# Kernel tuning notes

Measured on AMD Instinct MI355X. Metric: run time of the kernel, lower is better.

Reference implementation:

```python
import jax, jax.numpy as jnp
import numpy as np

STRIDES = (8, 16, 32)
BINS = 16
NC = 80
ALPHA, GAMMA = 0.25, 2.0
W_CLS, W_IOU, W_DFL = 1.0, 7.5, 1.5
B, MAX_GT = 32, 32
EPS = 1e-7


def setup_inputs() -> dict:
    key = jax.random.key(0)
    k0, k1, k2, k3, k4, k5, k6 = jax.random.split(key, 7)
    p0 = jax.random.normal(k0, (B, 4 * BINS + NC, 80, 80), dtype=jnp.float32)
    p1 = jax.random.normal(k1, (B, 4 * BINS + NC, 40, 40), dtype=jnp.float32)
    p2 = jax.random.normal(k2, (B, 4 * BINS + NC, 20, 20), dtype=jnp.float32)
    # realistic xyxy boxes inside a 640x640 image
    c = jax.random.uniform(k3, (B, MAX_GT, 2), minval=60.0, maxval=580.0)
    wh = jax.random.uniform(k4, (B, MAX_GT, 2), minval=16.0, maxval=120.0)
    gt_bboxes = jnp.concatenate([c - wh / 2, c + wh / 2], axis=-1).astype(jnp.float32)
    gt_labels = jax.random.randint(k5, (B, MAX_GT), 0, NC, dtype=jnp.int32)
    raw = jax.random.randint(k6, (B, 8400), 0, 20 * MAX_GT, dtype=jnp.int32)
    matched_gt_inds = jnp.where(raw < MAX_GT, raw, -1)
    return {"p0": p0, "p1": p1, "p2": p2, "gt_bboxes": gt_bboxes,
            "gt_labels": gt_labels, "matched_gt_inds": matched_gt_inds}


def _decode_scale(p, stride):
    # p: [B, 4*BINS + NC, H, W]
    Bp, C, H, W = p.shape
    dfl = p[:, :4 * BINS].reshape(Bp, 4, BINS, H, W)
    cls = p[:, 4 * BINS:]
    # DFL decode: expectation of softmax over bins, scaled by stride
    prob = jax.nn.softmax(dfl, axis=2)
    proj = jnp.arange(BINS, dtype=p.dtype)
    dist = jnp.einsum('bkchw,c->bkhw', prob, proj) * stride  # [B,4,H,W] in pixels
    ys, xs = jnp.meshgrid(jnp.arange(H), jnp.arange(W), indexing='ij')
    cx = ((xs.astype(p.dtype)) + 0.5) * stride
    cy = ((ys.astype(p.dtype)) + 0.5) * stride
    boxes = jnp.stack([cx - dist[:, 0], cy - dist[:, 1],
                       cx + dist[:, 2], cy + dist[:, 3]], axis=-1).reshape(Bp, H * W, 4)
    cls_logits = cls.transpose(0, 2, 3, 1).reshape(Bp, H * W, NC)
    dfl_flat = dfl.transpose(0, 3, 4, 1, 2).reshape(Bp, H * W, 4, BINS)
    grid = jnp.stack([cx, cy], axis=-1).reshape(H * W, 2)
    smap = jnp.full((H * W,), stride, dtype=p.dtype)
    return cls_logits, dfl_flat, boxes, grid, smap


def reference(p0, p1, p2, gt_bboxes, gt_labels, matched_gt_inds):
    outs = [_decode_scale(p, s) for p, s in zip((p0, p1, p2), STRIDES)]
    scores = jnp.concatenate([o[0] for o in outs], axis=1)   # [B,N,NC]
    dfl = jnp.concatenate([o[1] for o in outs], axis=1)      # [B,N,4,BINS]
    pboxes = jnp.concatenate([o[2] for o in outs], axis=1)   # [B,N,4]
    grid = jnp.concatenate([o[3] for o in outs], axis=0)     # [N,2]
    smap = jnp.concatenate([o[4] for o in outs], axis=0)     # [N]

    pos = matched_gt_inds >= 0                               # [B,N]
    idx = jnp.where(pos, matched_gt_inds, 0)
    lbl = jnp.take_along_axis(gt_labels, idx, axis=1)        # [B,N]
    posf = pos.astype(scores.dtype)
    tgt_scores = jax.nn.one_hot(lbl, NC, dtype=scores.dtype) * posf[..., None]

    # sigmoid focal loss (stable BCE-with-logits)
    prob = jax.nn.sigmoid(scores)
    ce = jnp.maximum(scores, 0) - scores * tgt_scores + jnp.log1p(jnp.exp(-jnp.abs(scores)))
    p_t = prob * tgt_scores + (1 - prob) * (1 - tgt_scores)
    alpha_t = tgt_scores * ALPHA + (1 - tgt_scores) * (1 - ALPHA)
    cls_elem = alpha_t * (1.0 - p_t) ** GAMMA * ce
    num_pos = jnp.maximum(posf.sum(), 1.0)
    loss_cls = cls_elem.sum() / num_pos

    # gather matched GT boxes per anchor
    tboxes = jnp.take_along_axis(gt_bboxes, idx[..., None], axis=1)  # [B,N,4]
    gx, gy = grid[None, :, 0], grid[None, :, 1]
    l = jnp.clip(gx - tboxes[..., 0], 0.0)
    t = jnp.clip(gy - tboxes[..., 1], 0.0)
    r = jnp.clip(tboxes[..., 2] - gx, 0.0)
    b_ = jnp.clip(tboxes[..., 3] - gy, 0.0)
    dists = jnp.stack([l, t, r, b_], axis=-1) / smap[None, :, None]   # [B,N,4]
    tb = jnp.clip(dists, 0.0, BINS - 1 - 1e-6)
    lo = jnp.floor(tb).astype(jnp.int32)
    hi = jnp.minimum(lo + 1, BINS - 1)
    a = tb - lo.astype(tb.dtype)
    # soft two-bin DFL target (vectorized form of the scatter_add loop)
    tdist = (jax.nn.one_hot(lo, BINS, dtype=dfl.dtype) * (1.0 - a)[..., None]
             + jax.nn.one_hot(hi, BINS, dtype=dfl.dtype) * a[..., None])   # [B,N,4,BINS]
    logp = jax.nn.log_softmax(dfl, axis=-1)
    dfl_elem = -(tdist * logp).sum(-1)                                # [B,N,4]
    loss_dfl = (dfl_elem * posf[..., None]).sum() / (num_pos * 4.0)

    # IoU loss on positives
    ix1 = jnp.maximum(pboxes[..., 0], tboxes[..., 0])
    iy1 = jnp.maximum(pboxes[..., 1], tboxes[..., 1])
    ix2 = jnp.minimum(pboxes[..., 2], tboxes[..., 2])
    iy2 = jnp.minimum(pboxes[..., 3], tboxes[..., 3])
    inter = jnp.clip(ix2 - ix1, 0.0) * jnp.clip(iy2 - iy1, 0.0)
    area_p = jnp.clip(pboxes[..., 2] - pboxes[..., 0], 0.0) * jnp.clip(pboxes[..., 3] - pboxes[..., 1], 0.0)
    area_t = jnp.clip(tboxes[..., 2] - tboxes[..., 0], 0.0) * jnp.clip(tboxes[..., 3] - tboxes[..., 1], 0.0)
    iou = inter / (area_p + area_t - inter + EPS)
    loss_iou = ((1.0 - iou) * posf).sum() / num_pos

    total = W_CLS * loss_cls + W_IOU * loss_iou + W_DFL * loss_dfl
    return total
```

## Files before the change

kernel.cpp:

```cpp
#include <hip/hip_runtime.h>
#include <math.h>

#define NCLS 80
#define BINS 16
#define BATCH 32
#define MAX_GT 32
#define NA 8400
#define AN (BATCH * NA)
#define NT 2100
#define NB_DFL 1050
#define NB_CLS 2560
#define NVB (NB_DFL + NB_CLS)
#define GRID 2048
#define NSLOT 64
#define ALPHA_C 0.25f
#define W_CLS 1.0
#define W_IOU 7.5
#define W_DFL 1.5
#define EPS_F 1e-7f

__device__ __forceinline__ float focal_elem(float s, float tt)
{
    float e   = __expf(-fabsf(s));
    float inv = 1.f / (1.f + e);
    float prob = (s >= 0.f) ? inv : e * inv;
    float ce  = fmaxf(s, 0.f) - s * tt + __logf(1.f + e);
    float p_t = prob * tt + (1.f - prob) * (1.f - tt);
    float alpha_t = tt * ALPHA_C + (1.f - tt) * (1.f - ALPHA_C);
    float om = 1.f - p_t;
    return alpha_t * om * om * ce;
}

__device__ __forceinline__ float focal0(float s)
{
    float e   = __expf(-fabsf(s));
    float inv = 1.f / (1.f + e);
    float prob = (s >= 0.f) ? inv : e * inv;
    float sp  = fmaxf(s, 0.f) + __logf(1.f + e);
    return 0.75f * prob * prob * sp;
}

__device__ __forceinline__ void block_write4(float c0, float c1, float c2, float c3,
                                             double* __restrict__ blk)
{
    #pragma unroll
    for (int o = 32; o > 0; o >>= 1) {
        c0 += __shfl_down(c0, o);
        c1 += __shfl_down(c1, o);
        c2 += __shfl_down(c2, o);
        c3 += __shfl_down(c3, o);
    }
    __shared__ float s4[4][4];
    const int wave = threadIdx.x >> 6, lane = threadIdx.x & 63;
    if (lane == 0) { s4[wave][0] = c0; s4[wave][1] = c1; s4[wave][2] = c2; s4[wave][3] = c3; }
    __syncthreads();
    if (threadIdx.x == 0) {
        double* o = blk + (size_t)blockIdx.x * 4;
        o[0] = (double)(s4[0][0] + s4[1][0] + s4[2][0] + s4[3][0]);
        o[1] = (double)(s4[0][1] + s4[1][1] + s4[2][1] + s4[3][1]);
        o[2] = (double)(s4[0][2] + s4[1][2] + s4[2][2] + s4[3][2]);
        o[3] = (double)(s4[0][3] + s4[1][3] + s4[2][3] + s4[3][3]);
    }
}

template<int HW, int SSTR, int WQ>
__device__ __forceinline__ void dfl_scale(
    const float* __restrict__ p, int b, int tl, int k, int gbase, int tid,
    const float* __restrict__ gt_bboxes, const int* __restrict__ gt_labels,
    const int* __restrict__ matched,
    float& c_cls, float& c_iou, float& c_dfl, float& c_cnt)
{
    const float stride = (float)SSTR;
    const float inv_s  = 1.f / stride;
    const int h  = tl / WQ;
    const int w0 = (tl - h * WQ) * 4;
    const int off = tl * 4;
    const float cy = ((float)h + 0.5f) * stride;
    const float* pc = p + (size_t)(b * 144 + k * BINS) * HW + off;

    const int4 m4 = *(const int4*)(matched + (size_t)b * NA + gbase + off);
    const int mm[4] = {m4.x, m4.y, m4.z, m4.w};

    float se[4] = {0.f, 0.f, 0.f, 0.f}, we[4] = {0.f, 0.f, 0.f, 0.f};
    #pragma unroll
    for (int i0 = 0; i0 < BINS; i0 += 4) {
        float4 qv[4];
        #pragma unroll
        for (int r = 0; r < 4; ++r)
            qv[r] = *(const float4*)(pc + (size_t)((i0 + r) * HW));
        #pragma unroll
        for (int r = 0; r < 4; ++r) {
            const float wgt = (float)(i0 + r);
            float e0 = __expf(qv[r].x), e1 = __expf(qv[r].y);
            float e2 = __expf(qv[r].z), e3 = __expf(qv[r].w);
            se[0] += e0; we[0] = fmaf(wgt, e0, we[0]);
            se[1] += e1; we[1] = fmaf(wgt, e1, we[1]);
            se[2] += e2; we[2] = fmaf(wgt, e2, we[2]);
            se[3] += e3; we[3] = fmaf(wgt, e3, we[3]);
        }
    }

    float pd[4];
    #pragma unroll
    for (int j = 0; j < 4; ++j) pd[j] = (we[j] / se[j]) * stride;

    #pragma unroll
    for (int j = 0; j < 4; ++j) {
        if (mm[j] >= 0) {
            const float4 tb = *(const float4*)(gt_bboxes + ((size_t)b * MAX_GT + mm[j]) * 4);
            const float cx = ((float)(w0 + j) + 0.5f) * stride;
            float d = (k == 0) ? (cx - tb.x) : (k == 1) ? (cy - tb.y)
                    : (k == 2) ? (tb.z - cx) : (tb.w - cy);
            float tval = fminf(fmaxf(d, 0.f) * inv_s, (float)(BINS - 1) - 1e-6f);
            int   lo = (int)tval;
            float fr = tval - (float)lo;
            float vlo = pc[(size_t)(lo * HW) + 0];
            float vhi = pc[(size_t)((lo + 1) * HW) + 0];
            vlo = pc[(size_t)(lo * HW) + j];
            vhi = pc[(size_t)((lo + 1) * HW) + j];
            float lse = __logf(se[j]);
            c_dfl += -((1.f - fr) * (vlo - lse) + fr * (vhi - lse));
        }
    }

    const int lbase = (tid & 63) & ~3;
    float d1[4], d2[4], d3[4];
    #pragma unroll
    for (int j = 0; j < 4; ++j) {
        d1[j] = __shfl(pd[j], lbase + 1);
        d2[j] = __shfl(pd[j], lbase + 2);
        d3[j] = __shfl(pd[j], lbase + 3);
    }
    if (k == 0) {
        #pragma unroll
        for (int j = 0; j < 4; ++j) {
            if (mm[j] >= 0) {
                const float cx = ((float)(w0 + j) + 0.5f) * stride;
                float px1 = cx - pd[j], py1 = cy - d1[j];
                float px2 = cx + d2[j], py2 = cy + d3[j];
                const float4 tb = *(const float4*)(gt_bboxes + ((size_t)b * MAX_GT + mm[j]) * 4);
                float ix1 = fmaxf(px1, tb.x), iy1 = fmaxf(py1, tb.y);
                float ix2 = fminf(px2, tb.z), iy2 = fminf(py2, tb.w);
                float inter  = fmaxf(ix2 - ix1, 0.f) * fmaxf(iy2 - iy1, 0.f);
                float area_p = fmaxf(px2 - px1, 0.f) * fmaxf(py2 - py1, 0.f);
                float area_t = fmaxf(tb.z - tb.x, 0.f) * fmaxf(tb.w - tb.y, 0.f);
                float iou = inter / (area_p + area_t - inter + EPS_F);
                c_iou += 1.f - iou;
                c_cnt += 1.f;
                int lbl = gt_labels[b * MAX_GT + mm[j]];
                float sv = *(p + (size_t)(b * 144 + 4 * BINS + lbl) * HW + off + j);
                c_cls += focal_elem(sv, 1.f) - focal_elem(sv, 0.f);
            }
        }
    }
}

__device__ __forceinline__ void cls_unit(int cvb, int tid,
    const float* __restrict__ p0, const float* __restrict__ p1,
    const float* __restrict__ p2, float& c_cls)
{
    const int b = cvb / NCLS;
    const int c = cvb - b * NCLS;
    const size_t cls_ch = (size_t)(b * 144 + 4 * BINS + c);

    float4 q[9];
    const float* pl0 = p0 + cls_ch * 6400;
    #pragma unroll
    for (int i = 0; i < 6; ++i) {
        int off = (i * 256 + tid) * 4;
        q[i] = *(const float4*)(pl0 + off);
    }
    #pragma unroll
    for (int i = 6; i < 9; ++i) {
        int t  = i * 256 + tid;
        int tc = (t < NT) ? t : 0;
        const float* p; int HW, off;
        if (tc < 1600)      { p = p0; HW = 6400; off = tc * 4; }
        else if (tc < 2000) { p = p1; HW = 1600; off = (tc - 1600) * 4; }
        else                { p = p2; HW = 400;  off = (tc - 2000) * 4; }
        q[i] = *(const float4*)(p + cls_ch * HW + off);
    }

    float part = 0.f;
    #pragma unroll
    for (int i = 0; i < 9; ++i) {
        const bool valid = (i < 8) || (i * 256 + tid < NT);
        float sum = focal0(q[i].x) + focal0(q[i].y) + focal0(q[i].z) + focal0(q[i].w);
        part += valid ? sum : 0.f;
    }
    c_cls += part;
}

__global__ __launch_bounds__(256) void yolo_mega(
    const float* __restrict__ p0, const float* __restrict__ p1, const float* __restrict__ p2,
    const float* __restrict__ gt_bboxes, const int* __restrict__ gt_labels,
    const int* __restrict__ matched, double* __restrict__ blk)
{
    const int tid = (int)threadIdx.x;
    float c_cls = 0.f, c_iou = 0.f, c_dfl = 0.f, c_cnt = 0.f;

    for (int vb = (int)blockIdx.x; vb < NVB; vb += GRID) {
        if (vb < NB_DFL) {
            const int gdt = vb * 256 + tid;
            const int k   = gdt & 3;
            const int qg  = gdt >> 2;
            const int b   = qg / NT;
            const int t   = qg - b * NT;
            if (t < 1600)
                dfl_scale<6400,  8, 20>(p0, b, t,        k, 0,    tid,
                                        gt_bboxes, gt_labels, matched, c_cls, c_iou, c_dfl, c_cnt);
            else if (t < 2000)
                dfl_scale<1600, 16, 10>(p1, b, t - 1600, k, 6400, tid,
                                        gt_bboxes, gt_labels, matched, c_cls, c_iou, c_dfl, c_cnt);
            else
                dfl_scale< 400, 32,  5>(p2, b, t - 2000, k, 8000, tid,
                                        gt_bboxes, gt_labels, matched, c_cls, c_iou, c_dfl, c_cnt);
        } else {
            cls_unit(vb - NB_DFL, tid, p0, p1, p2, c_cls);
        }
    }
    block_write4(c_cls, c_iou, c_dfl, c_cnt, blk);
}

__global__ __launch_bounds__(1024) void yolo_finalize_blocks(
    const double* __restrict__ blk, float* __restrict__ out)
{
    const int tid = (int)threadIdx.x;
    const double2* r0 = (const double2*)(blk + (size_t)tid * 4);
    const double2* r1 = (const double2*)(blk + (size_t)(tid + 1024) * 4);
    double2 a0 = r0[0], a1 = r0[1], b0 = r1[0], b1 = r1[1];
    double s0 = a0.x + b0.x, s1 = a0.y + b0.y, s2 = a1.x + b1.x, s3 = a1.y + b1.y;
    #pragma unroll
    for (int o = 32; o > 0; o >>= 1) {
        s0 += __shfl_down(s0, o); s1 += __shfl_down(s1, o);
        s2 += __shfl_down(s2, o); s3 += __shfl_down(s3, o);
    }
    __shared__ double sh[16][4];
    const int wave = tid >> 6, lane = tid & 63;
    if (lane == 0) { sh[wave][0] = s0; sh[wave][1] = s1; sh[wave][2] = s2; sh[wave][3] = s3; }
    __syncthreads();
    if (tid == 0) {
        double c = 0, i = 0, d = 0, n = 0;
        for (int w = 0; w < 16; ++w) { c += sh[w][0]; i += sh[w][1]; d += sh[w][2]; n += sh[w][3]; }
        double np = (n < 1.0) ? 1.0 : n;
        out[0] = (float)(W_CLS * c / np + W_IOU * i / np + W_DFL * d / (np * 4.0));
    }
}

__device__ __forceinline__ void block_reduce_atomic(float val, double* __restrict__ target)
{
    __shared__ float s[4];
    __syncthreads();
    #pragma unroll
    for (int o = 32; o > 0; o >>= 1) val += __shfl_down(val, o);
    const int wave = threadIdx.x >> 6, lane = threadIdx.x & 63;
    if (lane == 0) s[wave] = val;
    __syncthreads();
    if (threadIdx.x == 0) atomicAdd(target, (double)(s[0] + s[1] + s[2] + s[3]));
}

__global__ __launch_bounds__(256) void yolo_loss_fused(
    const float* __restrict__ p0, const float* __restrict__ p1, const float* __restrict__ p2,
    const float* __restrict__ gt_bboxes, const int* __restrict__ gt_labels,
    const int* __restrict__ matched, double* __restrict__ acc)
{
    const int a = blockIdx.x * blockDim.x + threadIdx.x;
    const int b = blockIdx.y;
    const int slot = blockIdx.x & (NSLOT - 1);
    float cls_acc = 0.f, iou_acc = 0.f, dfl_acc = 0.f, pos_cnt = 0.f;
    if (a < NA) {
        const float* p; int HW, W; float stride; int off;
        if (a < 6400)      { p = p0; HW = 6400; W = 80; stride = 8.f;  off = a; }
        else if (a < 8000) { p = p1; HW = 1600; W = 40; stride = 16.f; off = a - 6400; }
        else               { p = p2; HW = 400;  W = 20; stride = 32.f; off = a - 8000; }
        const int h = off / W, w = off - h * W;
        const float cx = ((float)w + 0.5f) * stride, cy = ((float)h + 0.5f) * stride;
        const float* pb = p + ((size_t)b * 144) * (size_t)HW + (size_t)off;
        const int m = matched[(size_t)b * NA + a];
        const bool pos = (m >= 0);
        const int idx = pos ? m : 0;
        const int lbl = gt_labels[b * MAX_GT + idx];
        const float* tbp = gt_bboxes + ((size_t)b * MAX_GT + idx) * 4;
        const float tx1 = tbp[0], ty1 = tbp[1], tx2 = tbp[2], ty2 = tbp[3];
        float tdist[4] = {fmaxf(cx - tx1, 0.f) / stride, fmaxf(cy - ty1, 0.f) / stride,
                          fmaxf(tx2 - cx, 0.f) / stride, fmaxf(ty2 - cy, 0.f) / stride};
        float pdv[4]; float dfl_sum = 0.f;
        #pragma unroll
        for (int k = 0; k < 4; ++k) {
            float tv = fminf(tdist[k], (float)(BINS - 1) - 1e-6f);
            int lo = (int)floorf(tv);
            float fr = tv - (float)lo;
            const float* pcx = pb + (size_t)(k * BINS) * HW;
            float v[BINS];
            #pragma unroll
            for (int i = 0; i < BINS; ++i) v[i] = pcx[(size_t)i * HW];
            float mx = v[0];
            #pragma unroll
            for (int i = 1; i < BINS; ++i) mx = fmaxf(mx, v[i]);
            float se = 0.f, we = 0.f, vlo = 0.f, vhi = 0.f;
            #pragma unroll
            for (int i = 0; i < BINS; ++i) {
                float e = __expf(v[i] - mx);
                se += e; we += (float)i * e;
                vlo = (i == lo) ? v[i] : vlo;
                vhi = (i == lo + 1) ? v[i] : vhi;
            }
            pdv[k] = (we / se) * stride;
            if (pos) { float lse = mx + __logf(se); dfl_sum += -((1.f - fr) * (vlo - lse) + fr * (vhi - lse)); }
        }
        const float* pcls = pb + (size_t)(4 * BINS) * HW;
        #pragma unroll 4
        for (int c = 0; c < NCLS; ++c)
            cls_acc += focal_elem(pcls[(size_t)c * HW], (pos && c == lbl) ? 1.f : 0.f);
        if (pos) {
            float px1 = cx - pdv[0], py1 = cy - pdv[1], px2 = cx + pdv[2], py2 = cy + pdv[3];
            float ix1 = fmaxf(px1, tx1), iy1 = fmaxf(py1, ty1);
            float ix2 = fminf(px2, tx2), iy2 = fminf(py2, ty2);
            float inter  = fmaxf(ix2 - ix1, 0.f) * fmaxf(iy2 - iy1, 0.f);
            float area_p = fmaxf(px2 - px1, 0.f) * fmaxf(py2 - py1, 0.f);
            float area_t = fmaxf(tx2 - tx1, 0.f) * fmaxf(ty2 - ty1, 0.f);
            float iou = inter / (area_p + area_t - inter + EPS_F);
            iou_acc = 1.f - iou; dfl_acc = dfl_sum; pos_cnt = 1.f;
        }
    }
    block_reduce_atomic(cls_acc, &acc[0 * NSLOT + slot]);
    block_reduce_atomic(iou_acc, &acc[1 * NSLOT + slot]);
    block_reduce_atomic(dfl_acc, &acc[2 * NSLOT + slot]);
    block_reduce_atomic(pos_cnt, &acc[3 * NSLOT + slot]);
}

__global__ void yolo_loss_finalize(const double* __restrict__ acc, float* __restrict__ out)
{
    double s[4] = {0.0, 0.0, 0.0, 0.0};
    for (int q = 0; q < 4; ++q)
        for (int i = 0; i < NSLOT; ++i) s[q] += acc[q * NSLOT + i];
    double np = s[3] < 1.0 ? 1.0 : s[3];
    double total = W_CLS * s[0] / np + W_IOU * s[1] / np + W_DFL * s[2] / (np * 4.0);
    out[0] = (float)total;
}

extern "C" void kernel_launch(void* const* d_in, const int* in_sizes, int n_in,
                              void* d_out, int out_size, void* d_ws, size_t ws_size,
                              hipStream_t stream)
{
    const float* p0        = (const float*)d_in[0];
    const float* p1        = (const float*)d_in[1];
    const float* p2        = (const float*)d_in[2];
    const float* gt_bboxes = (const float*)d_in[3];
    const int*   gt_labels = (const int*)d_in[4];
    const int*   matched   = (const int*)d_in[5];
    float*  out = (float*)d_out;

    const size_t need = (size_t)GRID * 4 * sizeof(double);

    if (ws_size >= need) {
        double* blk = (double*)d_ws;
        yolo_mega<<<GRID, 256, 0, stream>>>(p0, p1, p2, gt_bboxes, gt_labels, matched, blk);
        yolo_finalize_blocks<<<1, 1024, 0, stream>>>(blk, out);
    } else {
        double* acc = (double*)d_ws;
        (void)hipMemsetAsync(acc, 0, 4 * NSLOT * sizeof(double), stream);
        dim3 g((NA + 255) / 256, BATCH);
        yolo_loss_fused<<<g, 256, 0, stream>>>(p0, p1, p2, gt_bboxes, gt_labels, matched, acc);
        yolo_loss_finalize<<<1, 1, 0, stream>>>(acc, out);
    }
}
```

Before: 216.8 us.

## Restructure mega kernel to 128-thread blocks with contiguous class chunks and per-wave partials

```diff
diff --git a/kernel.cpp b/kernel.cpp
--- a/kernel.cpp
+++ b/kernel.cpp
@@ -8,10 +8,11 @@
 #define NA 8400
 #define AN (BATCH * NA)
 #define NT 2100
-#define NB_DFL 1050
-#define NB_CLS 2560
-#define NVB (NB_DFL + NB_CLS)
 #define GRID 2048
+#define NU_DFL 2100
+#define NU_CLS 5280
+#define NVB (NU_DFL + NU_CLS)
+#define NROWS (GRID * 2)
 #define NSLOT 64
 #define ALPHA_C 0.25f
 #define W_CLS 1.0
@@ -19,29 +20,26 @@
 #define W_DFL 1.5
 #define EPS_F 1e-7f
 
-__device__ __forceinline__ float focal_elem(float s, float tt)
-{
-    float e   = __expf(-fabsf(s));
-    float inv = 1.f / (1.f + e);
-    float prob = (s >= 0.f) ? inv : e * inv;
-    float ce  = fmaxf(s, 0.f) - s * tt + __logf(1.f + e);
-    float p_t = prob * tt + (1.f - prob) * (1.f - tt);
-    float alpha_t = tt * ALPHA_C + (1.f - tt) * (1.f - ALPHA_C);
-    float om = 1.f - p_t;
-    return alpha_t * om * om * ce;
-}
-
 __device__ __forceinline__ float focal0(float s)
 {
-    float e   = __expf(-fabsf(s));
-    float inv = 1.f / (1.f + e);
-    float prob = (s >= 0.f) ? inv : e * inv;
-    float sp  = fmaxf(s, 0.f) + __logf(1.f + e);
-    return 0.75f * prob * prob * sp;
-}
-
-__device__ __forceinline__ void block_write4(float c0, float c1, float c2, float c3,
-                                             double* __restrict__ blk)
+    float e  = __expf(-s);
+    float t  = 1.f + e;
+    float r  = __builtin_amdgcn_rcpf(t);
+    float lg = __logf(t);
+    return 0.75f * r * r * (s + lg);
+}
+
+__device__ __forceinline__ float focal_corr(float s)
+{
+    float e  = __expf(-s);
+    float t  = 1.f + e;
+    float r  = __builtin_amdgcn_rcpf(t);
+    float lg = __logf(t);
+    return r * r * (0.25f * e * e * lg - 0.75f * (s + lg));
+}
+
+__device__ __forceinline__ void wave_write4(float c0, float c1, float c2, float c3,
+                                            double* __restrict__ blk)
 {
     #pragma unroll
     for (int o = 32; o > 0; o >>= 1) {
@@ -50,16 +48,11 @@
         c2 += __shfl_down(c2, o);
         c3 += __shfl_down(c3, o);
     }
-    __shared__ float s4[4][4];
-    const int wave = threadIdx.x >> 6, lane = threadIdx.x & 63;
-    if (lane == 0) { s4[wave][0] = c0; s4[wave][1] = c1; s4[wave][2] = c2; s4[wave][3] = c3; }
-    __syncthreads();
-    if (threadIdx.x == 0) {
-        double* o = blk + (size_t)blockIdx.x * 4;
-        o[0] = (double)(s4[0][0] + s4[1][0] + s4[2][0] + s4[3][0]);
-        o[1] = (double)(s4[0][1] + s4[1][1] + s4[2][1] + s4[3][1]);
-        o[2] = (double)(s4[0][2] + s4[1][2] + s4[2][2] + s4[3][2]);
-        o[3] = (double)(s4[0][3] + s4[1][3] + s4[2][3] + s4[3][3]);
+    const int lane = (int)threadIdx.x & 63;
+    if (lane == 0) {
+        const int row = (int)blockIdx.x * 2 + ((int)threadIdx.x >> 6);
+        double* o = blk + (size_t)row * 4;
+        o[0] = (double)c0; o[1] = (double)c1; o[2] = (double)c2; o[3] = (double)c3;
     }
 }
 
@@ -78,26 +71,23 @@
     const float cy = ((float)h + 0.5f) * stride;
     const float* pc = p + (size_t)(b * 144 + k * BINS) * HW + off;
 
+    float4 v[BINS];
+    #pragma unroll
+    for (int i = 0; i < BINS; ++i)
+        v[i] = *(const float4*)(pc + (size_t)(i * HW));
     const int4 m4 = *(const int4*)(matched + (size_t)b * NA + gbase + off);
     const int mm[4] = {m4.x, m4.y, m4.z, m4.w};
 
     float se[4] = {0.f, 0.f, 0.f, 0.f}, we[4] = {0.f, 0.f, 0.f, 0.f};
     #pragma unroll
-    for (int i0 = 0; i0 < BINS; i0 += 4) {
-        float4 qv[4];
-        #pragma unroll
-        for (int r = 0; r < 4; ++r)
-            qv[r] = *(const float4*)(pc + (size_t)((i0 + r) * HW));
-        #pragma unroll
-        for (int r = 0; r < 4; ++r) {
-            const float wgt = (float)(i0 + r);
-            float e0 = __expf(qv[r].x), e1 = __expf(qv[r].y);
-            float e2 = __expf(qv[r].z), e3 = __expf(qv[r].w);
-            se[0] += e0; we[0] = fmaf(wgt, e0, we[0]);
-            se[1] += e1; we[1] = fmaf(wgt, e1, we[1]);
-            se[2] += e2; we[2] = fmaf(wgt, e2, we[2]);
-            se[3] += e3; we[3] = fmaf(wgt, e3, we[3]);
-        }
+    for (int i = 0; i < BINS; ++i) {
+        const float wgt = (float)i;
+        float e0 = __expf(v[i].x), e1 = __expf(v[i].y);
+        float e2 = __expf(v[i].z), e3 = __expf(v[i].w);
+        se[0] += e0; we[0] = fmaf(wgt, e0, we[0]);
+        se[1] += e1; we[1] = fmaf(wgt, e1, we[1]);
+        se[2] += e2; we[2] = fmaf(wgt, e2, we[2]);
+        se[3] += e3; we[3] = fmaf(wgt, e3, we[3]);
     }
 
     float pd[4];
@@ -114,10 +104,8 @@
             float tval = fminf(fmaxf(d, 0.f) * inv_s, (float)(BINS - 1) - 1e-6f);
             int   lo = (int)tval;
             float fr = tval - (float)lo;
-            float vlo = pc[(size_t)(lo * HW) + 0];
-            float vhi = pc[(size_t)((lo + 1) * HW) + 0];
-            vlo = pc[(size_t)(lo * HW) + j];
-            vhi = pc[(size_t)((lo + 1) * HW) + j];
+            float vlo = pc[(size_t)(lo * HW) + j];
+            float vhi = pc[(size_t)((lo + 1) * HW) + j];
             float lse = __logf(se[j]);
             c_dfl += -((1.f - fr) * (vlo - lse) + fr * (vhi - lse));
         }
@@ -149,49 +137,13 @@
                 c_cnt += 1.f;
                 int lbl = gt_labels[b * MAX_GT + mm[j]];
                 float sv = *(p + (size_t)(b * 144 + 4 * BINS + lbl) * HW + off + j);
-                c_cls += focal_elem(sv, 1.f) - focal_elem(sv, 0.f);
+                c_cls += focal_corr(sv);
             }
         }
     }
 }
 
-__device__ __forceinline__ void cls_unit(int cvb, int tid,
-    const float* __restrict__ p0, const float* __restrict__ p1,
-    const float* __restrict__ p2, float& c_cls)
-{
-    const int b = cvb / NCLS;
-    const int c = cvb - b * NCLS;
-    const size_t cls_ch = (size_t)(b * 144 + 4 * BINS + c);
-
-    float4 q[9];
-    const float* pl0 = p0 + cls_ch * 6400;
-    #pragma unroll
-    for (int i = 0; i < 6; ++i) {
-        int off = (i * 256 + tid) * 4;
-        q[i] = *(const float4*)(pl0 + off);
-    }
-    #pragma unroll
-    for (int i = 6; i < 9; ++i) {
-        int t  = i * 256 + tid;
-        int tc = (t < NT) ? t : 0;
-        const float* p; int HW, off;
-        if (tc < 1600)      { p = p0; HW = 6400; off = tc * 4; }
-        else if (tc < 2000) { p = p1; HW = 1600; off = (tc - 1600) * 4; }
-        else                { p = p2; HW = 400;  off = (tc - 2000) * 4; }
-        q[i] = *(const float4*)(p + cls_ch * HW + off);
-    }
-
-    float part = 0.f;
-    #pragma unroll
-    for (int i = 0; i < 9; ++i) {
-        const bool valid = (i < 8) || (i * 256 + tid < NT);
-        float sum = focal0(q[i].x) + focal0(q[i].y) + focal0(q[i].z) + focal0(q[i].w);
-        part += valid ? sum : 0.f;
-    }
-    c_cls += part;
-}
-
-__global__ __launch_bounds__(256) void yolo_mega(
+__global__ __launch_bounds__(128, 4) void yolo_mega(
     const float* __restrict__ p0, const float* __restrict__ p1, const float* __restrict__ p2,
     const float* __restrict__ gt_bboxes, const int* __restrict__ gt_labels,
     const int* __restrict__ matched, double* __restrict__ blk)
@@ -200,8 +152,8 @@
     float c_cls = 0.f, c_iou = 0.f, c_dfl = 0.f, c_cnt = 0.f;
 
     for (int vb = (int)blockIdx.x; vb < NVB; vb += GRID) {
-        if (vb < NB_DFL) {
-            const int gdt = vb * 256 + tid;
+        if (vb < NU_DFL) {
+            const int gdt = vb * 128 + tid;
             const int k   = gdt & 3;
             const int qg  = gdt >> 2;
             const int b   = qg / NT;
@@ -216,20 +168,44 @@
                 dfl_scale< 400, 32,  5>(p2, b, t - 2000, k, 8000, tid,
                                         gt_bboxes, gt_labels, matched, c_cls, c_iou, c_dfl, c_cnt);
         } else {
-            cls_unit(vb - NB_DFL, tid, p0, p1, p2, c_cls);
-        }
-    }
-    block_write4(c_cls, c_iou, c_dfl, c_cnt, blk);
+            const int c = vb - NU_DFL;
+            const int b = c / 165;
+            const int r = c - b * 165;
+            const float* base; int len, off;
+            if (r < 125)      { base = p0 + (size_t)b * 921600 + 409600; len = 512000; off = r * 4096; }
+            else if (r < 157) { base = p1 + (size_t)b * 230400 + 102400; len = 128000; off = (r - 125) * 4096; }
+            else              { base = p2 + (size_t)b * 57600  + 25600;  len = 32000;  off = (r - 157) * 4096; }
+
+            float4 q[8]; bool val[8];
+            #pragma unroll
+            for (int i = 0; i < 8; ++i) {
+                int o = off + i * 512 + tid * 4;
+                val[i] = (o < len);
+                q[i] = *(const float4*)(base + (val[i] ? o : 0));
+            }
+            float part = 0.f;
+            #pragma unroll
+            for (int i = 0; i < 8; ++i) {
+                float s = focal0(q[i].x) + focal0(q[i].y) + focal0(q[i].z) + focal0(q[i].w);
+                part += val[i] ? s : 0.f;
+            }
+            c_cls += part;
+        }
+    }
+    wave_write4(c_cls, c_iou, c_dfl, c_cnt, blk);
 }
 
 __global__ __launch_bounds__(1024) void yolo_finalize_blocks(
     const double* __restrict__ blk, float* __restrict__ out)
 {
     const int tid = (int)threadIdx.x;
-    const double2* r0 = (const double2*)(blk + (size_t)tid * 4);
-    const double2* r1 = (const double2*)(blk + (size_t)(tid + 1024) * 4);
-    double2 a0 = r0[0], a1 = r0[1], b0 = r1[0], b1 = r1[1];
-    double s0 = a0.x + b0.x, s1 = a0.y + b0.y, s2 = a1.x + b1.x, s3 = a1.y + b1.y;
+    double s0 = 0.0, s1 = 0.0, s2 = 0.0, s3 = 0.0;
+    #pragma unroll
+    for (int r = tid; r < NROWS; r += 1024) {
+        const double2* rp = (const double2*)(blk + (size_t)r * 4);
+        double2 a = rp[0], b = rp[1];
+        s0 += a.x; s1 += a.y; s2 += b.x; s3 += b.y;
+    }
     #pragma unroll
     for (int o = 32; o > 0; o >>= 1) {
         s0 += __shfl_down(s0, o); s1 += __shfl_down(s1, o);
@@ -257,6 +233,18 @@
     if (lane == 0) s[wave] = val;
     __syncthreads();
     if (threadIdx.x == 0) atomicAdd(target, (double)(s[0] + s[1] + s[2] + s[3]));
+}
+
+__device__ __forceinline__ float focal_elem(float s, float tt)
+{
+    float e   = __expf(-fabsf(s));
+    float inv = 1.f / (1.f + e);
+    float prob = (s >= 0.f) ? inv : e * inv;
+    float ce  = fmaxf(s, 0.f) - s * tt + __logf(1.f + e);
+    float p_t = prob * tt + (1.f - prob) * (1.f - tt);
+    float alpha_t = tt * ALPHA_C + (1.f - tt) * (1.f - ALPHA_C);
+    float om = 1.f - p_t;
+    return alpha_t * om * om * ce;
 }
 
 __global__ __launch_bounds__(256) void yolo_loss_fused(
@@ -351,11 +339,11 @@
     const int*   matched   = (const int*)d_in[5];
     float*  out = (float*)d_out;
 
-    const size_t need = (size_t)GRID * 4 * sizeof(double);
+    const size_t need = (size_t)NROWS * 4 * sizeof(double);
 
     if (ws_size >= need) {
         double* blk = (double*)d_ws;
-        yolo_mega<<<GRID, 256, 0, stream>>>(p0, p1, p2, gt_bboxes, gt_labels, matched, blk);
+        yolo_mega<<<GRID, 128, 0, stream>>>(p0, p1, p2, gt_bboxes, gt_labels, matched, blk);
         yolo_finalize_blocks<<<1, 1024, 0, stream>>>(blk, out);
     } else {
         double* acc = (double*)d_ws;
```

New measurement: 219.0 us. No clear change (+1.1%).
